# Performance work log

Measured on AMD Instinct MI355X. Metric: run time of the kernel, lower is better.

Reference implementation:

```python
import jax, jax.numpy as jnp
import numpy as np

SERIES_LEN = 4096
D_EMB = 1024
D_V = 1024
HURST = 0.7
H = HURST - 0.5          # exponent used by the module
DT = 1.0 / SERIES_LEN
EPS = 1e-8


def _attn_matrix():
    # Lower-triangular fractional power-law matrix A2[i, j]:
    #   j <  i : ((i - j) * dt + 1e-8) ** (hurst - 0.5)
    #   j == i : 1e-8 ** (hurst - 0.5)
    #   j >  i : 0
    i = jnp.arange(SERIES_LEN, dtype=jnp.int32)[:, None]
    j = jnp.arange(SERIES_LEN, dtype=jnp.int32)[None, :]
    diff = jnp.clip(i - j, 1, None).astype(jnp.float32)  # safe base for fractional power
    lower = jnp.where(i > j, (diff * DT + EPS) ** H, 0.0)
    diag = jnp.eye(SERIES_LEN, dtype=jnp.float32) * (EPS ** H)
    return lower + diag  # (L, L) float32


def setup_inputs() -> dict:
    key = jax.random.key(0)
    k1, k2 = jax.random.split(key)
    embed_series = jax.random.normal(k1, (D_EMB, SERIES_LEN), dtype=jnp.float32)
    # nn.Linear(d_emb, d_v, bias=False) weight has shape (d_v, d_emb)
    Wv_weight = jax.random.normal(k2, (D_V, D_EMB), dtype=jnp.float32) * (1.0 / np.sqrt(D_EMB))
    return {"embed_series": embed_series, "Wv_weight": Wv_weight}


def reference(embed_series, Wv_weight):
    # V (original, d_v x L) = Wv(embed_series.T).T ; output[i, c] = sum_j A2[i, j] * V[c, j]
    # => out = A2 @ (embed_series.T @ Wv_weight.T), shape (L, d_v)
    A2 = _attn_matrix()                                   # (L, L) lower triangular
    Y = jnp.einsum('el,ve->lv', embed_series, Wv_weight)  # (L, d_v)
    return A2 @ Y                                         # (L, d_v)
```

## Files before the change

kernel.cpp:

```cpp
#include <hip/hip_runtime.h>
#include <hip/hip_bf16.h>
#include <cstdint>
#include <cstddef>


#define L_SER 4096
#define DEMB  1024
#define DV    1024

#define R_STRIDE 4224
#define R_O0     4096

typedef __bf16 bf16_t;
typedef __attribute__((ext_vector_type(8))) __bf16 bf16x8;
typedef __attribute__((ext_vector_type(4))) float f32x4;

__device__ __forceinline__ void glds16(const bf16_t* g, bf16_t* l) {
    __builtin_amdgcn_global_load_lds(
        (const __attribute__((address_space(1))) unsigned int*)(const void*)g,
        (__attribute__((address_space(3))) unsigned int*)(void*)l,
        16, 0, 0);
}

__global__ void prep_kernel(const float* __restrict__ E, const float* __restrict__ W,
                            bf16_t* __restrict__ Eb, bf16_t* __restrict__ Wb,
                            bf16_t* __restrict__ R) {
    const int b = blockIdx.x;
    if (b < 132) {
        int idx = b * 256 + threadIdx.x;
        int s = idx / R_STRIDE;
        int x = idx - s * R_STRIDE;
        int d = R_O0 + s - x;
        float v = 0.0f;
        if (d >= 0 && d < L_SER)
            v = powf((d == 0) ? 1e-8f : ((float)d * (1.0f / (float)L_SER) + 1e-8f), 0.2f);
        R[idx] = (bf16_t)v;
    } else if (b < 132 + 2048) {
        int idx = (b - 132) * 256 + threadIdx.x;
        const f32x4* s = (const f32x4*)E;
        f32x4 v0 = s[idx * 2], v1 = s[idx * 2 + 1];
        bf16x8 o;
        o[0] = (bf16_t)v0[0]; o[1] = (bf16_t)v0[1]; o[2] = (bf16_t)v0[2]; o[3] = (bf16_t)v0[3];
        o[4] = (bf16_t)v1[0]; o[5] = (bf16_t)v1[1]; o[6] = (bf16_t)v1[2]; o[7] = (bf16_t)v1[3];
        ((bf16x8*)Eb)[idx] = o;
    } else {
        int idx = (b - 2180) * 256 + threadIdx.x;
        const f32x4* s = (const f32x4*)W;
        f32x4 v0 = s[idx * 2], v1 = s[idx * 2 + 1];
        bf16x8 o;
        o[0] = (bf16_t)v0[0]; o[1] = (bf16_t)v0[1]; o[2] = (bf16_t)v0[2]; o[3] = (bf16_t)v0[3];
        o[4] = (bf16_t)v1[0]; o[5] = (bf16_t)v1[1]; o[6] = (bf16_t)v1[2]; o[7] = (bf16_t)v1[3];
        ((bf16x8*)Wb)[idx] = o;
    }
}

__global__ void tsum_kernel(const bf16_t* __restrict__ T0, const bf16_t* __restrict__ T1,
                            bf16_t* __restrict__ Tsum) {
    int idx = blockIdx.x * 256 + threadIdx.x;
    bf16x8 t0 = ((const bf16x8*)T0)[idx];
    bf16x8 t1 = ((const bf16x8*)T1)[idx];
    bf16x8 o;
#pragma unroll
    for (int u = 0; u < 8; ++u) o[u] = (bf16_t)((float)t0[u] + (float)t1[u]);
    ((bf16x8*)Tsum)[idx] = o;
}

#define GA_STAGE(SBOFS)                                                      \
    _Pragma("unroll")                                                        \
    for (int c = 0; c < 4; ++c) {                                            \
        glds16(pA[c], &sA[(SBOFS) + (c * 32 + wave * 8) * 64]);              \
        glds16(pB[c], &sB[(SBOFS) + (c * 32 + wave * 8) * 64]);              \
        pA[c] += 64; pB[c] += 64;                                            \
    }

#define GA_COMPUTE(SBOFS)                                                    \
    _Pragma("unroll")                                                        \
    for (int kk = 0; kk < 2; ++kk) {                                         \
        const int co = kk ? coff1 : coff0;                                   \
        bf16x8 afr[4], bfr[4];                                               \
        _Pragma("unroll")                                                    \
        for (int tm = 0; tm < 4; ++tm)                                       \
            afr[tm] = *(const bf16x8*)&sA[(SBOFS) + (wm * 64 + tm * 16 + ln) * 64 + co]; \
        _Pragma("unroll")                                                    \
        for (int tn = 0; tn < 4; ++tn)                                       \
            bfr[tn] = *(const bf16x8*)&sB[(SBOFS) + (wn * 64 + tn * 16 + ln) * 64 + co]; \
        _Pragma("unroll")                                                    \
        for (int tm = 0; tm < 4; ++tm)                                       \
            _Pragma("unroll")                                                \
            for (int tn = 0; tn < 4; ++tn)                                   \
                acc[tm][tn] = __builtin_amdgcn_mfma_f32_16x16x32_bf16(afr[tm], bfr[tn], acc[tm][tn], 0, 0, 0); \
    }

#define GA_LANES()                                                           \
    const int tid  = threadIdx.x;                                            \
    const int wave = tid >> 6;                                               \
    const int lane = tid & 63;                                               \
    const int quad = lane >> 4;                                              \
    const int ln   = lane & 15;                                              \
    const int wm   = wave >> 1;                                              \
    const int wn   = wave & 1;                                               \
    const int lrow = lane >> 3;                                              \
    const int lch  = (lane & 7) ^ lrow;                                      \
    const int rsw   = ln & 7;                                                \
    const int coff0 = ((quad ^ rsw)) * 8;                                    \
    const int coff1 = (((4 + quad) ^ rsw)) * 8;

#define GA_LOOP()                                                            \
    GA_STAGE(0)                                                              \
    for (int s = 0;; s += 2) {                                               \
        __syncthreads();                                                     \
        if (s + 1 < nsteps) { GA_STAGE(128 * 64) }                           \
        GA_COMPUTE(0)                                                        \
        if (s + 1 >= nsteps) break;                                          \
        __syncthreads();                                                     \
        if (s + 2 < nsteps) { GA_STAGE(0) }                                  \
        GA_COMPUTE(128 * 64)                                                 \
        if (s + 2 >= nsteps) break;                                          \
    }

__global__ __launch_bounds__(256, 2) void gemm_a_kernel(const bf16_t* __restrict__ R,
                                                        const bf16_t* __restrict__ Eb,
                                                        bf16_t* __restrict__ T0,
                                                        bf16_t* __restrict__ T1) {
    __shared__ __align__(16) bf16_t sA[2 * 128 * 64];
    __shared__ __align__(16) bf16_t sB[2 * 128 * 64];

    const int bid = blockIdx.x;
    int I, nb, h;
    if (bid < 256) { I = bid >> 3;                nb = bid & 7;         h = 0; }
    else           { I = 31 - ((bid - 256) >> 3); nb = (bid - 256) & 7; h = 1; }
    const int i0 = I * 128;
    const int n0 = nb * 128;
    const int nsteps = I + 1;
    const int j0b = h ? 64 * (I + 1) : 0;
    bf16_t* __restrict__ Tout = h ? T1 : T0;

    GA_LANES()

    f32x4 acc[4][4];
#pragma unroll
    for (int a = 0; a < 4; ++a)
#pragma unroll
        for (int b = 0; b < 4; ++b) acc[a][b] = (f32x4){0, 0, 0, 0};

    const bf16_t* pA[4];
    const bf16_t* pB[4];
#pragma unroll
    for (int c = 0; c < 4; ++c) {
        int r = c * 32 + wave * 8 + lrow;
        pA[c] = R + (size_t)(r & 7) * R_STRIDE + (R_O0 - i0 + j0b - 8 * (r >> 3) + lch * 8);
        pB[c] = Eb + (size_t)(n0 + r) * L_SER + j0b + lch * 8;
    }

    GA_LOOP()

#pragma unroll
    for (int tm = 0; tm < 4; ++tm) {
        int row_base = i0 + wm * 64 + tm * 16 + quad * 4;
#pragma unroll
        for (int tn = 0; tn < 4; ++tn) {
            int col = n0 + wn * 64 + tn * 16 + ln;
#pragma unroll
            for (int r = 0; r < 4; ++r)
                Tout[(size_t)(row_base + r) * DEMB + col] = (bf16_t)acc[tm][tn][r];
        }
    }
}

__global__ __launch_bounds__(256, 2) void gemm_b_kernel(const bf16_t* __restrict__ Tsum,
                                                        const bf16_t* __restrict__ Wb,
                                                        float* __restrict__ out) {
    __shared__ __align__(16) bf16_t sA[2 * 128 * 64];
    __shared__ __align__(16) bf16_t sB[2 * 128 * 64];

    const int bid = blockIdx.x;
    const int ib = bid >> 3;
    const int nb = bid & 7;
    const int i0 = ib * 128;
    const int n0 = nb * 128;

    GA_LANES()

    f32x4 acc[4][4];
#pragma unroll
    for (int a = 0; a < 4; ++a)
#pragma unroll
        for (int b = 0; b < 4; ++b) acc[a][b] = (f32x4){0, 0, 0, 0};

    const int nsteps = DEMB / 64;

    const bf16_t* pA[4];
    const bf16_t* pB[4];
#pragma unroll
    for (int c = 0; c < 4; ++c) {
        int r = c * 32 + wave * 8 + lrow;
        pA[c] = Tsum + (size_t)(i0 + r) * DEMB + lch * 8;
        pB[c] = Wb + (size_t)(n0 + r) * DEMB + lch * 8;
    }

    GA_LOOP()

#pragma unroll
    for (int tm = 0; tm < 4; ++tm) {
        int row_base = i0 + wm * 64 + tm * 16 + quad * 4;
#pragma unroll
        for (int tn = 0; tn < 4; ++tn) {
            int col = n0 + wn * 64 + tn * 16 + ln;
#pragma unroll
            for (int r = 0; r < 4; ++r)
                out[(size_t)(row_base + r) * DV + col] = acc[tm][tn][r];
        }
    }
}

extern "C" void kernel_launch(void* const* d_in, const int* in_sizes, int n_in,
                              void* d_out, int out_size, void* d_ws, size_t ws_size,
                              hipStream_t stream) {
    const float* E = (const float*)d_in[0];
    const float* W = (const float*)d_in[1];
    float* out = (float*)d_out;

    char* ws = (char*)d_ws;
    bf16_t* Eb   = (bf16_t*)(ws);
    bf16_t* T0   = (bf16_t*)(ws + (size_t)8  * 1024 * 1024);
    bf16_t* T1   = (bf16_t*)(ws + (size_t)16 * 1024 * 1024);
    bf16_t* Tsum = (bf16_t*)(ws + (size_t)24 * 1024 * 1024);
    bf16_t* Wb   = (bf16_t*)(ws + (size_t)32 * 1024 * 1024);
    bf16_t* R    = (bf16_t*)(ws + (size_t)34 * 1024 * 1024);

    prep_kernel<<<2692, 256, 0, stream>>>(E, W, Eb, Wb, R);
    gemm_a_kernel<<<512, 256, 0, stream>>>(R, Eb, T0, T1);
    tsum_kernel<<<2048, 256, 0, stream>>>(T0, T1, Tsum);
    gemm_b_kernel<<<256, 256, 0, stream>>>(Tsum, Wb, out);
}
```

Baseline: 129.3 us.

## Fuse T0+T1 summation into second GEMM by stacking halves along K

Drops the separate elementwise kernel that summed the two partial results of the first GEMM into a bf16 buffer. The second GEMM now loads 64-row tiles from both T0 and T1 into one 128-row shared tile and sends both halves through the MFMA into the same accumulators. This removes one kernel launch and a full read/write pass of the intermediate. The price is double the loads of Wb per output and a grid of 512 blocks with half-size output tiles, which gives more blocks and less reuse per block.

```diff
diff --git a/kernel.cpp b/kernel.cpp
--- a/kernel.cpp
+++ b/kernel.cpp
@@ -54,17 +54,6 @@
     }
 }
 
-__global__ void tsum_kernel(const bf16_t* __restrict__ T0, const bf16_t* __restrict__ T1,
-                            bf16_t* __restrict__ Tsum) {
-    int idx = blockIdx.x * 256 + threadIdx.x;
-    bf16x8 t0 = ((const bf16x8*)T0)[idx];
-    bf16x8 t1 = ((const bf16x8*)T1)[idx];
-    bf16x8 o;
-#pragma unroll
-    for (int u = 0; u < 8; ++u) o[u] = (bf16_t)((float)t0[u] + (float)t1[u]);
-    ((bf16x8*)Tsum)[idx] = o;
-}
-
 #define GA_STAGE(SBOFS)                                                      \
     _Pragma("unroll")                                                        \
     for (int c = 0; c < 4; ++c) {                                            \
@@ -105,19 +94,6 @@
     const int coff0 = ((quad ^ rsw)) * 8;                                    \
     const int coff1 = (((4 + quad) ^ rsw)) * 8;
 
-#define GA_LOOP()                                                            \
-    GA_STAGE(0)                                                              \
-    for (int s = 0;; s += 2) {                                               \
-        __syncthreads();                                                     \
-        if (s + 1 < nsteps) { GA_STAGE(128 * 64) }                           \
-        GA_COMPUTE(0)                                                        \
-        if (s + 1 >= nsteps) break;                                          \
-        __syncthreads();                                                     \
-        if (s + 2 < nsteps) { GA_STAGE(0) }                                  \
-        GA_COMPUTE(128 * 64)                                                 \
-        if (s + 2 >= nsteps) break;                                          \
-    }
-
 __global__ __launch_bounds__(256, 2) void gemm_a_kernel(const bf16_t* __restrict__ R,
                                                         const bf16_t* __restrict__ Eb,
                                                         bf16_t* __restrict__ T0,
@@ -152,7 +128,17 @@
         pB[c] = Eb + (size_t)(n0 + r) * L_SER + j0b + lch * 8;
     }
 
-    GA_LOOP()
+    GA_STAGE(0)
+    for (int s = 0;; s += 2) {
+        __syncthreads();
+        if (s + 1 < nsteps) { GA_STAGE(128 * 64) }
+        GA_COMPUTE(0)
+        if (s + 1 >= nsteps) break;
+        __syncthreads();
+        if (s + 2 < nsteps) { GA_STAGE(0) }
+        GA_COMPUTE(128 * 64)
+        if (s + 2 >= nsteps) break;
+    }
 
 #pragma unroll
     for (int tm = 0; tm < 4; ++tm) {
@@ -167,7 +153,31 @@
     }
 }
 
-__global__ __launch_bounds__(256, 2) void gemm_b_kernel(const bf16_t* __restrict__ Tsum,
+#define GB_COMPUTE(SBOFS)                                                    \
+    _Pragma("unroll")                                                        \
+    for (int kk = 0; kk < 2; ++kk) {                                         \
+        const int co = kk ? coff1 : coff0;                                   \
+        bf16x8 afr[4], bfr[4];                                               \
+        _Pragma("unroll")                                                    \
+        for (int c = 0; c < 4; ++c)                                          \
+            afr[c] = *(const bf16x8*)&sA[(SBOFS) + (((c >> 1) * 64) + wm * 32 + (c & 1) * 16 + ln) * 64 + co]; \
+        _Pragma("unroll")                                                    \
+        for (int tn = 0; tn < 4; ++tn)                                       \
+            bfr[tn] = *(const bf16x8*)&sB[(SBOFS) + (wn * 64 + tn * 16 + ln) * 64 + co]; \
+        _Pragma("unroll")                                                    \
+        for (int t = 0; t < 2; ++t)                                          \
+            _Pragma("unroll")                                                \
+            for (int tn = 0; tn < 4; ++tn)                                   \
+                acc[t][tn] = __builtin_amdgcn_mfma_f32_16x16x32_bf16(afr[t], bfr[tn], acc[t][tn], 0, 0, 0); \
+        _Pragma("unroll")                                                    \
+        for (int t = 0; t < 2; ++t)                                          \
+            _Pragma("unroll")                                                \
+            for (int tn = 0; tn < 4; ++tn)                                   \
+                acc[t][tn] = __builtin_amdgcn_mfma_f32_16x16x32_bf16(afr[2 + t], bfr[tn], acc[t][tn], 0, 0, 0); \
+    }
+
+__global__ __launch_bounds__(256, 2) void gemm_b_kernel(const bf16_t* __restrict__ T0,
+                                                        const bf16_t* __restrict__ T1,
                                                         const bf16_t* __restrict__ Wb,
                                                         float* __restrict__ out) {
     __shared__ __align__(16) bf16_t sA[2 * 128 * 64];
@@ -176,14 +186,14 @@
     const int bid = blockIdx.x;
     const int ib = bid >> 3;
     const int nb = bid & 7;
-    const int i0 = ib * 128;
+    const int i0 = ib * 64;
     const int n0 = nb * 128;
 
     GA_LANES()
 
-    f32x4 acc[4][4];
-#pragma unroll
-    for (int a = 0; a < 4; ++a)
+    f32x4 acc[2][4];
+#pragma unroll
+    for (int a = 0; a < 2; ++a)
 #pragma unroll
         for (int b = 0; b < 4; ++b) acc[a][b] = (f32x4){0, 0, 0, 0};
 
@@ -193,22 +203,33 @@
     const bf16_t* pB[4];
 #pragma unroll
     for (int c = 0; c < 4; ++c) {
-        int r = c * 32 + wave * 8 + lrow;
-        pA[c] = Tsum + (size_t)(i0 + r) * DEMB + lch * 8;
-        pB[c] = Wb + (size_t)(n0 + r) * DEMB + lch * 8;
-    }
-
-    GA_LOOP()
-
-#pragma unroll
-    for (int tm = 0; tm < 4; ++tm) {
-        int row_base = i0 + wm * 64 + tm * 16 + quad * 4;
+        const bf16_t* base = (c < 2) ? T0 : T1;
+        int rr = (c & 1) * 32 + wave * 8 + lrow;
+        pA[c] = base + (size_t)(i0 + rr) * DEMB + lch * 8;
+        pB[c] = Wb + (size_t)(n0 + c * 32 + wave * 8 + lrow) * DEMB + lch * 8;
+    }
+
+    GA_STAGE(0)
+    for (int s = 0;; s += 2) {
+        __syncthreads();
+        if (s + 1 < nsteps) { GA_STAGE(128 * 64) }
+        GB_COMPUTE(0)
+        if (s + 1 >= nsteps) break;
+        __syncthreads();
+        if (s + 2 < nsteps) { GA_STAGE(0) }
+        GB_COMPUTE(128 * 64)
+        if (s + 2 >= nsteps) break;
+    }
+
+#pragma unroll
+    for (int t = 0; t < 2; ++t) {
+        int row_base = i0 + wm * 32 + t * 16 + quad * 4;
 #pragma unroll
         for (int tn = 0; tn < 4; ++tn) {
             int col = n0 + wn * 64 + tn * 16 + ln;
 #pragma unroll
             for (int r = 0; r < 4; ++r)
-                out[(size_t)(row_base + r) * DV + col] = acc[tm][tn][r];
+                out[(size_t)(row_base + r) * DV + col] = acc[t][tn][r];
         }
     }
 }
@@ -221,15 +242,13 @@
     float* out = (float*)d_out;
 
     char* ws = (char*)d_ws;
-    bf16_t* Eb   = (bf16_t*)(ws);
-    bf16_t* T0   = (bf16_t*)(ws + (size_t)8  * 1024 * 1024);
-    bf16_t* T1   = (bf16_t*)(ws + (size_t)16 * 1024 * 1024);
-    bf16_t* Tsum = (bf16_t*)(ws + (size_t)24 * 1024 * 1024);
-    bf16_t* Wb   = (bf16_t*)(ws + (size_t)32 * 1024 * 1024);
-    bf16_t* R    = (bf16_t*)(ws + (size_t)34 * 1024 * 1024);
+    bf16_t* Eb = (bf16_t*)(ws);
+    bf16_t* T0 = (bf16_t*)(ws + (size_t)8  * 1024 * 1024);
+    bf16_t* T1 = (bf16_t*)(ws + (size_t)16 * 1024 * 1024);
+    bf16_t* Wb = (bf16_t*)(ws + (size_t)24 * 1024 * 1024);
+    bf16_t* R  = (bf16_t*)(ws + (size_t)26 * 1024 * 1024);
 
     prep_kernel<<<2692, 256, 0, stream>>>(E, W, Eb, Wb, R);
     gemm_a_kernel<<<512, 256, 0, stream>>>(R, Eb, T0, T1);
-    tsum_kernel<<<2048, 256, 0, stream>>>(T0, T1, Tsum);
-    gemm_b_kernel<<<256, 256, 0, stream>>>(Tsum, Wb, out);
-}
+    gemm_b_kernel<<<512, 256, 0, stream>>>(T0, T1, Wb, out);
+}
```

New measurement: 125.0 us. -3.3%, faster.
